# Optimization experiments

Measured on AMD Instinct MI355X. Metric: run time of the kernel, lower is better.

The kernel has to match this reference:

```python
import jax, jax.numpy as jnp
import numpy as np
from math import sqrt

BASE = 10000.0  # rope_theta
NUM_HEADS = 16


def _quant(x):
    # per-row (last-dim) symmetric int8 fake-quant, matching ActivationQuantSTE.forward
    scale = 127.0 / jnp.maximum(jnp.max(jnp.abs(x), axis=-1, keepdims=True), 1e-5)
    return jnp.clip(jnp.round(x * scale), -128.0, 127.0) / scale


@jax.custom_vjp
def act_quant(x):
    return _quant(x)

def _aq_fwd(x):
    return _quant(x), None

def _aq_bwd(_, g):
    return (g,)  # straight-through estimator

act_quant.defvjp(_aq_fwd, _aq_bwd)


def complex_linear(xr, xi, Wr, Wi):
    # ComplexLinearBase: quantize activations, then
    #   y_real = q_real @ Wr^T + q_imag @ Wi^T
    #   y_imag = q_real @ Wi^T - q_imag @ Wr^T
    qr = act_quant(xr)
    qi = act_quant(xi)
    yr = qr @ Wr.T + qi @ Wi.T
    yi = qr @ Wi.T - qi @ Wr.T
    return yr, yi


def setup_inputs() -> dict:
    T, H = 2048, 2048
    key = jax.random.key(0)
    ks = jax.random.split(key, 10)
    w = lambda k: jax.random.normal(k, (H, H), jnp.float32) * 0.02
    return {
        "hidden_real": jax.random.normal(ks[0], (T, H), jnp.float32),
        "hidden_imag": jax.random.normal(ks[1], (T, H), jnp.float32),
        "positions": jnp.arange(T, dtype=jnp.int32),
        "Wq_r": w(ks[2]), "Wq_i": w(ks[3]),
        "Wk_r": w(ks[4]), "Wk_i": w(ks[5]),
        "Wv_r": w(ks[6]), "Wv_i": w(ks[7]),
        "Wo_r": w(ks[8]), "Wo_i": w(ks[9]),
    }


def reference(hidden_real, hidden_imag, positions, Wq_r, Wq_i, Wk_r, Wk_i, Wv_r, Wv_i, Wo_r, Wo_i):
    T, H = hidden_real.shape
    NH = NUM_HEADS
    D = H // NH  # head_dim

    # complex QKV projections with int8 activation fake-quant
    qr, qi = complex_linear(hidden_real, hidden_imag, Wq_r, Wq_i)
    kr, ki = complex_linear(hidden_real, hidden_imag, Wk_r, Wk_i)
    vr, vi = complex_linear(hidden_real, hidden_imag, Wv_r, Wv_i)

    # Complex RoPE: interleaving (real, imag) then GPT-J-style rotation with
    # head_size = rotary_dim = 2*D is equivalent to rotating (real, imag) pairs:
    #   out_real = real*cos - imag*sin ; out_imag = imag*cos + real*sin
    # inv_freq = base^-(arange(0, 2D, 2)/(2D)) = base^-(arange(D)/D), len D.
    inv_freq = 1.0 / (BASE ** (jnp.arange(D, dtype=jnp.float32) / D))
    freqs = positions.astype(jnp.float32)[:, None] * inv_freq[None, :]  # [T, D]
    # cache is stored in bf16 in the original module
    cos = jnp.cos(freqs).astype(jnp.bfloat16).astype(jnp.float32)[:, None, :]  # [T,1,D]
    sin = jnp.sin(freqs).astype(jnp.bfloat16).astype(jnp.float32)[:, None, :]

    def rope(xr_, xi_):
        r = xr_.reshape(T, NH, D)
        i = xi_.reshape(T, NH, D)
        return r * cos - i * sin, i * cos + r * sin

    qr3, qi3 = rope(qr, qi)
    kr3, ki3 = rope(kr, ki)
    vr3 = vr.reshape(T, NH, D)
    vi3 = vi.reshape(T, NH, D)

    # causal attention; scores = Re(q . conj(k)) / sqrt(2*D)  (complex dim is 2*D)
    scale = 1.0 / sqrt(2 * D)
    scores = (jnp.einsum('thd,shd->hts', qr3, kr3)
              + jnp.einsum('thd,shd->hts', qi3, ki3)) * scale  # [NH, T, T]
    causal = jnp.tril(jnp.ones((T, T), dtype=bool))
    scores = jnp.where(causal[None], scores, -1e9)
    p = jax.nn.softmax(scores, axis=-1)

    out_r = jnp.einsum('hts,shd->thd', p, vr3).reshape(T, H)
    out_i = jnp.einsum('hts,shd->thd', p, vi3).reshape(T, H)

    # complex output projection (with activation fake-quant)
    return complex_linear(out_r, out_i, Wo_r, Wo_i)
```

## Files before the change

kernel.cpp:

```cpp
#include <hip/hip_runtime.h>


typedef float v4f __attribute__((ext_vector_type(4)));
typedef _Float16 v8h __attribute__((ext_vector_type(8)));
typedef _Float16 v4h __attribute__((ext_vector_type(4)));

typedef const __attribute__((address_space(1))) void glob_void;
typedef __attribute__((address_space(3))) void lds_void;

__device__ __forceinline__ void gload16(const _Float16* gp, _Float16* lp) {
  __builtin_amdgcn_global_load_lds((glob_void*)gp, (lds_void*)lp, 16, 0, 0);
}

__device__ __forceinline__ float bf16_rt(float f) {
  union { float f; unsigned u; } a; a.f = f;
  unsigned r = (a.u + 0x7fffu + ((a.u >> 16) & 1u)) & 0xffff0000u;
  union { unsigned u; float f; } b; b.u = r;
  return b.f;
}

#define EPI_QKV 0
#define EPI_OUT 1

#define SBAR()  __builtin_amdgcn_sched_barrier(0)
#define WBAR()  __builtin_amdgcn_s_barrier()
#define LGKM0() asm volatile("s_waitcnt lgkmcnt(0)" ::: "memory")

__global__ __launch_bounds__(512, 2) void gemm_qkv256(
    const _Float16* __restrict__ A, const _Float16* __restrict__ B,
    _Float16* __restrict__ Yq, _Float16* __restrict__ vt)
{
  const int p = blockIdx.x;
  const int xcd = p & 7, s = p >> 3;
  const int mt = s & 7, ntl = s >> 3;
  const int nt = xcd * 8 + ntl;
  const int m0 = mt << 8;
  const int n0 = nt * 192;

  __shared__ __align__(16) _Float16 lds[57344];

  const int tid = threadIdx.x, lane = tid & 63, wave = tid >> 6;
  const int quad = lane >> 4, l15 = lane & 15;
  const int wm = wave >> 2, wn = wave & 3;

  const int rr = tid >> 2;
  const int lc8 = (((tid & 3) ^ ((tid >> 3) & 3)) << 3);
  const _Float16* gA = A + (long long)(m0 + rr) * 4096 + lc8;
  const _Float16* gBj[3];
#pragma unroll
  for (int j = 0; j < 3; ++j) {
    const int ks = (j == 2) || (j == 1 && tid >= 256);
    const int r = j * 128 + (tid >> 2) - ks * 192;
    gBj[j] = B + (long long)(n0 + r) * 4096 + ks * 32 + lc8;
  }

  const int co = ((quad ^ ((l15 >> 1) & 3)) << 3);
  const int aBase = (wm * 128 + l15) * 32 + co;
  const int bBase = (wn * 48 + l15) * 32 + co;

  v4f acc[8][3] = {};

  {
    _Float16* sd = lds + tid * 8;
    gload16(gA, sd);
    gload16(gA + 524288, sd + 4096);
    gload16(gBj[0], sd + 16384);
    gload16(gBj[1], sd + 20480);
    gload16(gA + 32, sd + 8192);
    gload16(gA + 524288 + 32, sd + 12288);
    gload16(gBj[2], sd + 24576);
  }
  asm volatile("s_waitcnt vmcnt(3)" ::: "memory");
  WBAR();

  for (int t = 0; t < 64; ++t) {
    const _Float16* As = lds + (t & 1) * 28672;
    const _Float16* Bs = As + 16384;
    _Float16* sd = lds + ((t & 1) ^ 1) * 28672 + tid * 8;
    const int k1 = (t + 1) << 6;
    const bool stg = (t < 63);

    v8h bf[3], af[4];

    af[0] = *(const v8h*)&As[aBase];
    af[1] = *(const v8h*)&As[aBase + 512];
    af[2] = *(const v8h*)&As[aBase + 1024];
    af[3] = *(const v8h*)&As[aBase + 1536];
    bf[0] = *(const v8h*)&Bs[bBase];
    bf[1] = *(const v8h*)&Bs[bBase + 512];
    bf[2] = *(const v8h*)&Bs[bBase + 1024];
    if (stg) { gload16(gA + k1, sd); gload16(gA + k1 + 524288, sd + 4096); }
    SBAR(); WBAR(); LGKM0(); SBAR();
    __builtin_amdgcn_s_setprio(1);
#pragma unroll
    for (int i = 0; i < 4; ++i)
#pragma unroll
      for (int nf = 0; nf < 3; ++nf)
        acc[i][nf] = __builtin_amdgcn_mfma_f32_16x16x32_f16(af[i], bf[nf], acc[i][nf], 0, 0, 0);
    __builtin_amdgcn_s_setprio(0);
    WBAR();

    af[0] = *(const v8h*)&As[aBase + 2048];
    af[1] = *(const v8h*)&As[aBase + 2560];
    af[2] = *(const v8h*)&As[aBase + 3072];
    af[3] = *(const v8h*)&As[aBase + 3584];
    if (stg) { gload16(gBj[0] + k1, sd + 16384); gload16(gBj[1] + k1, sd + 20480); }
    SBAR(); WBAR(); LGKM0(); SBAR();
    __builtin_amdgcn_s_setprio(1);
#pragma unroll
    for (int i = 0; i < 4; ++i)
#pragma unroll
      for (int nf = 0; nf < 3; ++nf)
        acc[4 + i][nf] = __builtin_amdgcn_mfma_f32_16x16x32_f16(af[i], bf[nf], acc[4 + i][nf], 0, 0, 0);
    __builtin_amdgcn_s_setprio(0);
    if (stg) asm volatile("s_waitcnt vmcnt(4)" ::: "memory");
    else     asm volatile("s_waitcnt vmcnt(0)" ::: "memory");
    WBAR();

    bf[0] = *(const v8h*)&Bs[bBase + 6144];
    bf[1] = *(const v8h*)&Bs[bBase + 6656];
    bf[2] = *(const v8h*)&Bs[bBase + 7168];
    af[0] = *(const v8h*)&As[aBase + 8192];
    af[1] = *(const v8h*)&As[aBase + 8704];
    af[2] = *(const v8h*)&As[aBase + 9216];
    af[3] = *(const v8h*)&As[aBase + 9728];
    if (stg) { gload16(gA + k1 + 32, sd + 8192); gload16(gA + k1 + 524288 + 32, sd + 12288); }
    SBAR(); WBAR(); LGKM0(); SBAR();
    __builtin_amdgcn_s_setprio(1);
#pragma unroll
    for (int i = 0; i < 4; ++i)
#pragma unroll
      for (int nf = 0; nf < 3; ++nf)
        acc[i][nf] = __builtin_amdgcn_mfma_f32_16x16x32_f16(af[i], bf[nf], acc[i][nf], 0, 0, 0);
    __builtin_amdgcn_s_setprio(0);
    WBAR();

    af[0] = *(const v8h*)&As[aBase + 10240];
    af[1] = *(const v8h*)&As[aBase + 10752];
    af[2] = *(const v8h*)&As[aBase + 11264];
    af[3] = *(const v8h*)&As[aBase + 11776];
    if (stg) gload16(gBj[2] + k1, sd + 24576);
    SBAR(); WBAR(); LGKM0(); SBAR();
    __builtin_amdgcn_s_setprio(1);
#pragma unroll
    for (int i = 0; i < 4; ++i)
#pragma unroll
      for (int nf = 0; nf < 3; ++nf)
        acc[4 + i][nf] = __builtin_amdgcn_mfma_f32_16x16x32_f16(af[i], bf[nf], acc[4 + i][nf], 0, 0, 0);
    __builtin_amdgcn_s_setprio(0);
    if (stg) asm volatile("s_waitcnt vmcnt(3)" ::: "memory");
    WBAR();
  }

#pragma unroll
  for (int mf = 0; mf < 8; ++mf) {
#pragma unroll
    for (int nf = 0; nf < 3; ++nf) {
      const int col = n0 + wn * 48 + nf * 16 + l15;
      const int row0 = m0 + wm * 128 + mf * 16 + quad * 4;
      if (col >= 8192) {
        const int c = col - 8192;
        const int hh = (c & 2047) >> 7;
        const int dcol = (c < 2048) ? (c & 127) : (128 + (c & 127));
        v4h pk;
#pragma unroll
        for (int r = 0; r < 4; ++r) pk[r] = (_Float16)acc[mf][nf][r];
        *(v4h*)(vt + ((long long)(hh * 256 + dcol)) * 2048 + row0) = pk;
      } else {
#pragma unroll
        for (int r = 0; r < 4; ++r)
          Yq[(long long)(row0 + r) * 8192 + col] = (_Float16)acc[mf][nf][r];
      }
    }
  }
}

template<int EPI>
__global__ __launch_bounds__(256) void gemm_nt(
    const _Float16* __restrict__ A, const _Float16* __restrict__ B,
    void* __restrict__ Cv, int K, int lda, int ldb, int ldc,
    _Float16* __restrict__ vtout)
{
  const int m0 = blockIdx.x * 128, n0 = blockIdx.y * 128;

  __shared__ __align__(16) _Float16 As[128 * 32];
  __shared__ __align__(16) _Float16 Bs[128 * 32];

  const int tid = threadIdx.x, lane = tid & 63, wave = tid >> 6;
  const int off0 = tid * 8, off1 = 2048 + tid * 8;
  const int r0 = off0 >> 5, r1 = off1 >> 5;
  const int c0 = ((((off0 >> 3) & 3) ^ ((r0 >> 1) & 3)) << 3);
  const int c1 = ((((off1 >> 3) & 3) ^ ((r1 >> 1) & 3)) << 3);
  const _Float16* ga0 = A + (long long)(m0 + r0) * lda + c0;
  const _Float16* ga1 = A + (long long)(m0 + r1) * lda + c1;
  const _Float16* gb0 = B + (long long)(n0 + r0) * ldb + c0;
  const _Float16* gb1 = B + (long long)(n0 + r1) * ldb + c1;

  const int mr = (wave >> 1) * 64 + (lane & 15);
  const int nr = (wave & 1) * 64 + (lane & 15);
  const int kq = lane >> 4;

  v4f acc[4][4] = {};

  for (int k0 = 0; k0 < K; k0 += 32) {
    gload16(ga0 + k0, As + off0);
    gload16(ga1 + k0, As + off1);
    gload16(gb0 + k0, Bs + off0);
    gload16(gb1 + k0, Bs + off1);
    __syncthreads();
    v8h a[4], b[4];
#pragma unroll
    for (int i = 0; i < 4; ++i) {
      const int r = mr + i * 16;
      a[i] = *(const v8h*)&As[r * 32 + ((kq ^ ((r >> 1) & 3)) << 3)];
    }
#pragma unroll
    for (int j = 0; j < 4; ++j) {
      const int r = nr + j * 16;
      b[j] = *(const v8h*)&Bs[r * 32 + ((kq ^ ((r >> 1) & 3)) << 3)];
    }
#pragma unroll
    for (int i = 0; i < 4; ++i)
#pragma unroll
      for (int j = 0; j < 4; ++j)
        acc[i][j] = __builtin_amdgcn_mfma_f32_16x16x32_f16(a[i], b[j], acc[i][j], 0, 0, 0);
    __syncthreads();
  }

  const int cr = (wave >> 1) * 64 + (lane >> 4) * 4;
  const int cc = (wave & 1) * 64 + (lane & 15);
#pragma unroll
  for (int i = 0; i < 4; ++i)
#pragma unroll
    for (int j = 0; j < 4; ++j) {
      const int col = n0 + cc + j * 16;
      if (EPI == EPI_QKV && col >= 8192) {
        const int c = col - 8192;
        const int hh = (c & 2047) >> 7;
        const int dcol = (c < 2048) ? (c & 127) : (128 + (c & 127));
        const int row0 = m0 + cr + i * 16;
        v4h pk;
#pragma unroll
        for (int r = 0; r < 4; ++r) pk[r] = (_Float16)acc[i][j][r];
        *(v4h*)(vtout + ((long long)(hh * 256 + dcol)) * 2048 + row0) = pk;
      } else {
#pragma unroll
        for (int r = 0; r < 4; ++r) {
          const int row = m0 + cr + i * 16 + r;
          const float v = acc[i][j][r];
          if (EPI == EPI_QKV) {
            ((_Float16*)Cv)[(long long)row * ldc + col] = (_Float16)v;
          } else {
            float* O = (float*)Cv;
            if (col < 2048) O[(long long)row * 2048 + col] = v;
            else O[2048ll * 2048 + (long long)row * 2048 + (col - 2048)] = v;
          }
        }
      }
    }
}

__global__ __launch_bounds__(256) void quant_rows(
    const float* __restrict__ s0, const float* __restrict__ s1,
    _Float16* __restrict__ dst)
{
  const int t = blockIdx.x, y = blockIdx.y;
  const float* src = (y ? s1 : s0) + (long long)t * 2048;
  const int tid = threadIdx.x, lane = tid & 63, wave = tid >> 6;
  __shared__ float rbuf[4];
  const v4f a = *(const v4f*)(src + tid * 4);
  const v4f b = *(const v4f*)(src + 1024 + tid * 4);
  float m = 0.f;
#pragma unroll
  for (int k = 0; k < 4; ++k)
    m = fmaxf(m, fmaxf(fabsf(a[k]), fabsf(b[k])));
  for (int o = 1; o < 64; o <<= 1) m = fmaxf(m, __shfl_xor(m, o, 64));
  if (lane == 0) rbuf[wave] = m;
  __syncthreads();
  m = fmaxf(fmaxf(rbuf[0], rbuf[1]), fmaxf(rbuf[2], rbuf[3]));
  const float scale = 127.f / fmaxf(m, 1e-5f);
  const float inv = 1.f / scale;
  _Float16* d = dst + (long long)t * 4096 + (long long)y * 2048 + tid * 4;
  v4h qa, qb;
#pragma unroll
  for (int k = 0; k < 4; ++k) {
    qa[k] = (_Float16)(fminf(fmaxf(rintf(a[k] * scale), -128.f), 127.f) * inv);
    qb[k] = (_Float16)(fminf(fmaxf(rintf(b[k] * scale), -128.f), 127.f) * inv);
  }
  *(v4h*)d = qa;
  *(v4h*)(d + 1024) = qb;
}

__global__ __launch_bounds__(256) void wprep(
    const float* __restrict__ Wq_r, const float* __restrict__ Wq_i,
    const float* __restrict__ Wk_r, const float* __restrict__ Wk_i,
    const float* __restrict__ Wv_r, const float* __restrict__ Wv_i,
    const float* __restrict__ Wo_r, const float* __restrict__ Wo_i,
    _Float16* __restrict__ Bqkv, _Float16* __restrict__ Bo)
{
  const float* Ws[8] = {Wq_r, Wq_i, Wk_r, Wk_i, Wv_r, Wv_i, Wo_r, Wo_i};
  const int i = blockIdx.x * 256 + threadIdx.x;
  const int w = i >> 18;
  const int rem = i & 262143;
  const int j = rem >> 7;
  const int cb = (rem & 127) * 16;
  const float* src = Ws[w] + (long long)j * 2048 + cb;
  _Float16* Bp = (w < 6) ? (Bqkv + (long long)(w >> 1) * 4096 * 4096) : Bo;
  const int isI = w & 1;
  _Float16* d1 = Bp + (long long)j * 4096 + (isI ? 2048 + cb : cb);
  _Float16* d2 = Bp + (long long)(2048 + j) * 4096 + (isI ? cb : 2048 + cb);
  const float sg2 = isI ? 1.f : -1.f;
#pragma unroll
  for (int q = 0; q < 4; ++q) {
    const v4f v = *(const v4f*)(src + q * 4);
    v4h o1, o2;
#pragma unroll
    for (int k = 0; k < 4; ++k) {
      o1[k] = (_Float16)v[k];
      o2[k] = (_Float16)(v[k] * sg2);
    }
    *(v4h*)(d1 + q * 4) = o1;
    *(v4h*)(d2 + q * 4) = o2;
  }
}

__global__ __launch_bounds__(256) void trig_kernel(
    const int* __restrict__ pos, float* __restrict__ cs)
{
  const int t = blockIdx.x * 2 + (threadIdx.x >> 7);
  const int d = threadIdx.x & 127;
  const float invf = (float)pow(10000.0, -(double)d / 128.0);
  const float fr = (float)pos[t] * invf;
  const double fd = (double)fr;
  cs[((long long)t * 128 + d) * 2]     = bf16_rt((float)cos(fd));
  cs[((long long)t * 128 + d) * 2 + 1] = bf16_rt((float)sin(fd));
}

__global__ __launch_bounds__(256) void rope_kernel(
    const _Float16* __restrict__ Yq, const float* __restrict__ cs,
    _Float16* __restrict__ qc, _Float16* __restrict__ kc)
{
  const int idx = blockIdx.x * 256 + threadIdx.x;
  const int d0 = (idx & 15) * 8;
  const int h  = (idx >> 4) & 15;
  const int t  = idx >> 8;
  const _Float16* y = Yq + (long long)t * 8192 + h * 128 + d0;
  const v8h qr8 = *(const v8h*)(y);
  const v8h qi8 = *(const v8h*)(y + 2048);
  const v8h kr8 = *(const v8h*)(y + 4096);
  const v8h ki8 = *(const v8h*)(y + 6144);
  const float* cp = cs + ((long long)t * 128 + d0) * 2;
  v8h qro, qio, kro, kio;
#pragma unroll
  for (int u = 0; u < 8; ++u) {
    const float c = cp[u * 2], s = cp[u * 2 + 1];
    const float qr = (float)qr8[u], qi = (float)qi8[u];
    const float kr = (float)kr8[u], ki = (float)ki8[u];
    qro[u] = (_Float16)(qr * c - qi * s);
    qio[u] = (_Float16)(qi * c + qr * s);
    kro[u] = (_Float16)(kr * c - ki * s);
    kio[u] = (_Float16)(ki * c + kr * s);
  }
  _Float16* qo = qc + ((long long)h * 2048 + t) * 256 + d0;
  _Float16* ko = kc + ((long long)h * 2048 + t) * 256 + d0;
  *(v8h*)qo = qro; *(v8h*)(qo + 128) = qio;
  *(v8h*)ko = kro; *(v8h*)(ko + 128) = kio;
}

__global__ __launch_bounds__(256, 4) void flash_attn(
    const _Float16* __restrict__ qc, const _Float16* __restrict__ kc,
    const _Float16* __restrict__ vt, float* __restrict__ attn)
{
  __shared__ __align__(16) _Float16 Ps[32 * 72];
  __shared__ float pmax[2][32];
  __shared__ float psum[2][32];

  const int h  = blockIdx.y;
  const int qt = ((h >> 3) & 1) ? (63 - (int)blockIdx.x) : (int)blockIdx.x;
  const int q0 = qt * 32;
  const int tid = threadIdx.x, lane = tid & 63, wave = tid >> 6;
  const int mi = wave >> 1, ni = wave & 1;
  const int quad = lane >> 4, l15 = lane & 15;

  const _Float16* qh = qc + (long long)h * 2048 * 256;
  const _Float16* kh = kc + (long long)h * 2048 * 256;
  const _Float16* vh = vt + (long long)h * 256 * 2048;

  const _Float16 scl = (_Float16)0.09016844f;
  v8h qf[8];
  {
    const int t = q0 + mi * 16 + l15;
#pragma unroll
    for (int ks = 0; ks < 8; ++ks) {
      v8h q = *(const v8h*)(qh + (long long)t * 256 + ks * 32 + quad * 8);
#pragma unroll
      for (int u = 0; u < 8; ++u) q[u] *= scl;
      qf[ks] = q;
    }
  }

  float mrow[4], lrow[4];
  v4f acc_o[8];
#pragma unroll
  for (int r = 0; r < 4; ++r) { mrow[r] = -1e30f; lrow[r] = 0.f; }
#pragma unroll
  for (int nt = 0; nt < 8; ++nt) acc_o[nt] = (v4f){0.f, 0.f, 0.f, 0.f};

  const int stmax = qt >> 1;
  for (int st = 0; st <= stmax; ++st) {
    const int s0 = st * 64;

    v4f sa[2] = {};
#pragma unroll
    for (int ks = 0; ks < 8; ++ks) {
      v8h bk[2];
#pragma unroll
      for (int jn = 0; jn < 2; ++jn)
        bk[jn] = *(const v8h*)(kh + (long long)(s0 + ni * 32 + jn * 16 + l15) * 256
                               + ks * 32 + quad * 8);
#pragma unroll
      for (int jn = 0; jn < 2; ++jn)
        sa[jn] = __builtin_amdgcn_mfma_f32_16x16x32_f16(qf[ks], bk[jn], sa[jn], 0, 0, 0);
    }

    const bool diag = (st == stmax);
    float pm[4];
#pragma unroll
    for (int r = 0; r < 4; ++r) pm[r] = -1e30f;
#pragma unroll
    for (int jn = 0; jn < 2; ++jn)
#pragma unroll
      for (int r = 0; r < 4; ++r) {
        float v = sa[jn][r];
        if (diag) {
          const int rl = q0 + mi * 16 + quad * 4 + r;
          const int cl = s0 + ni * 32 + jn * 16 + l15;
          if (cl > rl) v = -1e30f;
        }
        sa[jn][r] = v;
        pm[r] = fmaxf(pm[r], v);
      }
#pragma unroll
    for (int o = 1; o < 16; o <<= 1)
#pragma unroll
      for (int r = 0; r < 4; ++r)
        pm[r] = fmaxf(pm[r], __shfl_xor(pm[r], o, 64));
    if (l15 == 0) {
#pragma unroll
      for (int r = 0; r < 4; ++r)
        pmax[ni][mi * 16 + quad * 4 + r] = pm[r];
    }
    __syncthreads();

    float al[4], ps[4];
#pragma unroll
    for (int r = 0; r < 4; ++r) {
      const int row = mi * 16 + quad * 4 + r;
      const float mn = fmaxf(mrow[r], fmaxf(pmax[0][row], pmax[1][row]));
      al[r] = __builtin_amdgcn_exp2f(mrow[r] - mn);
      mrow[r] = mn;
      ps[r] = 0.f;
    }
#pragma unroll
    for (int jn = 0; jn < 2; ++jn)
#pragma unroll
      for (int r = 0; r < 4; ++r) {
        const float e = __builtin_amdgcn_exp2f(sa[jn][r] - mrow[r]);
        ps[r] += e;
        Ps[(mi * 16 + quad * 4 + r) * 72 + ni * 32 + jn * 16 + l15] = (_Float16)e;
      }
#pragma unroll
    for (int o = 1; o < 16; o <<= 1)
#pragma unroll
      for (int r = 0; r < 4; ++r)
        ps[r] += __shfl_xor(ps[r], o, 64);
    if (l15 == 0) {
#pragma unroll
      for (int r = 0; r < 4; ++r)
        psum[ni][mi * 16 + quad * 4 + r] = ps[r];
    }
    __syncthreads();

#pragma unroll
    for (int r = 0; r < 4; ++r) {
      const int row = mi * 16 + quad * 4 + r;
      lrow[r] = lrow[r] * al[r] + psum[0][row] + psum[1][row];
    }
#pragma unroll
    for (int nt = 0; nt < 8; ++nt)
#pragma unroll
      for (int r = 0; r < 4; ++r)
        acc_o[nt][r] *= al[r];

#pragma unroll
    for (int kc2 = 0; kc2 < 2; ++kc2) {
      v8h pa;
      {
        const int row = mi * 16 + l15;
        pa = *(const v8h*)(Ps + row * 72 + kc2 * 32 + quad * 8);
      }
#pragma unroll
      for (int nt = 0; nt < 8; ++nt) {
        const v8h vb = *(const v8h*)(vh + (long long)(ni * 128 + nt * 16 + l15) * 2048
                                     + s0 + kc2 * 32 + quad * 8);
        acc_o[nt] = __builtin_amdgcn_mfma_f32_16x16x32_f16(pa, vb, acc_o[nt], 0, 0, 0);
      }
    }
  }

  float inv[4];
#pragma unroll
  for (int r = 0; r < 4; ++r) inv[r] = 1.f / lrow[r];
#pragma unroll
  for (int nt = 0; nt < 8; ++nt) {
    const int d = ni * 128 + nt * 16 + l15;
    float* dst = attn + ((d < 128) ? 0ll : (2048ll * 2048)) + (h * 128 + (d & 127));
#pragma unroll
    for (int r = 0; r < 4; ++r) {
      const int t = q0 + mi * 16 + quad * 4 + r;
      dst[(long long)t * 2048] = acc_o[nt][r] * inv[r];
    }
  }
}

extern "C" void kernel_launch(void* const* d_in, const int* in_sizes, int n_in,
                              void* d_out, int out_size, void* d_ws, size_t ws_size,
                              hipStream_t stream) {
  const float* hr   = (const float*)d_in[0];
  const float* hi   = (const float*)d_in[1];
  const int*   pos  = (const int*)d_in[2];
  const float* Wq_r = (const float*)d_in[3];
  const float* Wq_i = (const float*)d_in[4];
  const float* Wk_r = (const float*)d_in[5];
  const float* Wk_i = (const float*)d_in[6];
  const float* Wv_r = (const float*)d_in[7];
  const float* Wv_i = (const float*)d_in[8];
  const float* Wo_r = (const float*)d_in[9];
  const float* Wo_i = (const float*)d_in[10];

  char* ws = (char*)d_ws;
  _Float16* Bqkv = (_Float16*)(ws);
  float*    attn = (float*)   (ws);
  float*    cs   = (float*)   (ws + (32ll  << 20));
  _Float16* Bo   = (_Float16*)(ws + (96ll  << 20));
  _Float16* Ac   = (_Float16*)(ws + (128ll << 20));
  _Float16* Yq   = (_Float16*)(ws + (144ll << 20));
  _Float16* qc   = (_Float16*)(ws + (176ll << 20));
  _Float16* kc   = (_Float16*)(ws + (192ll << 20));
  _Float16* vt   = (_Float16*)(ws + (208ll << 20));

  quant_rows<<<dim3(2048, 2), 256, 0, stream>>>(hr, hi, Ac);
  wprep<<<8192, 256, 0, stream>>>(Wq_r, Wq_i, Wk_r, Wk_i, Wv_r, Wv_i, Wo_r, Wo_i, Bqkv, Bo);
  gemm_qkv256<<<512, 512, 0, stream>>>(Ac, Bqkv, Yq, vt);
  trig_kernel<<<1024, 256, 0, stream>>>(pos, cs);
  rope_kernel<<<2048, 256, 0, stream>>>(Yq, cs, qc, kc);
  flash_attn<<<dim3(64, 16), 256, 0, stream>>>(qc, kc, vt, attn);
  quant_rows<<<dim3(2048, 2), 256, 0, stream>>>(attn, attn + 2048ll * 2048, Ac);
  gemm_nt<EPI_OUT><<<dim3(16, 32), 256, 0, stream>>>(
      Ac, Bo, d_out, 4096, 4096, 4096, 0, nullptr);
}
```

Measured before the change: 838.9 us.

## Restructure flash attention so each wave owns full rows, removing block syncs

Flash attention now uses a 64-row query tile per block with each of the four waves owning 16 query rows across the full 64-key tile and all 256 head dims. This removes the cross-wave max/sum exchange through LDS and both __syncthreads per key tile, since row statistics are reduced within a wave. Each wave now issues twice the K loads and MFMAs per tile and holds 16 output accumulators, so register pressure rises and the occupancy hint drops from 4 to 2. The grid halves to 512 blocks. s_setprio hints are also added around the MFMA bursts.

```diff
diff --git a/kernel.cpp b/kernel.cpp
--- a/kernel.cpp
+++ b/kernel.cpp
@@ -367,29 +367,28 @@
   *(v8h*)ko = kro; *(v8h*)(ko + 128) = kio;
 }
 
-__global__ __launch_bounds__(256, 4) void flash_attn(
+__global__ __launch_bounds__(256, 2) void flash_attn(
     const _Float16* __restrict__ qc, const _Float16* __restrict__ kc,
     const _Float16* __restrict__ vt, float* __restrict__ attn)
 {
-  __shared__ __align__(16) _Float16 Ps[32 * 72];
-  __shared__ float pmax[2][32];
-  __shared__ float psum[2][32];
+  __shared__ __align__(16) _Float16 Ps[4][16][72];
 
   const int h  = blockIdx.y;
-  const int qt = ((h >> 3) & 1) ? (63 - (int)blockIdx.x) : (int)blockIdx.x;
-  const int q0 = qt * 32;
+  const int qt = ((h >> 3) & 1) ? (31 - (int)blockIdx.x) : (int)blockIdx.x;
+  const int q0 = qt * 64;
   const int tid = threadIdx.x, lane = tid & 63, wave = tid >> 6;
-  const int mi = wave >> 1, ni = wave & 1;
   const int quad = lane >> 4, l15 = lane & 15;
 
   const _Float16* qh = qc + (long long)h * 2048 * 256;
   const _Float16* kh = kc + (long long)h * 2048 * 256;
   const _Float16* vh = vt + (long long)h * 256 * 2048;
 
+  const int wrow = q0 + wave * 16;
+
   const _Float16 scl = (_Float16)0.09016844f;
   v8h qf[8];
   {
-    const int t = q0 + mi * 16 + l15;
+    const int t = wrow + l15;
 #pragma unroll
     for (int ks = 0; ks < 8; ++ks) {
       v8h q = *(const v8h*)(qh + (long long)t * 256 + ks * 32 + quad * 8);
@@ -400,41 +399,42 @@
   }
 
   float mrow[4], lrow[4];
-  v4f acc_o[8];
+  v4f acc_o[16];
 #pragma unroll
   for (int r = 0; r < 4; ++r) { mrow[r] = -1e30f; lrow[r] = 0.f; }
 #pragma unroll
-  for (int nt = 0; nt < 8; ++nt) acc_o[nt] = (v4f){0.f, 0.f, 0.f, 0.f};
-
-  const int stmax = qt >> 1;
-  for (int st = 0; st <= stmax; ++st) {
+  for (int nt = 0; nt < 16; ++nt) acc_o[nt] = (v4f){0.f, 0.f, 0.f, 0.f};
+
+  for (int st = 0; st <= qt; ++st) {
     const int s0 = st * 64;
-
-    v4f sa[2] = {};
+    const bool diag = (st == qt);
+
+    v4f sa[4] = {};
 #pragma unroll
     for (int ks = 0; ks < 8; ++ks) {
-      v8h bk[2];
-#pragma unroll
-      for (int jn = 0; jn < 2; ++jn)
-        bk[jn] = *(const v8h*)(kh + (long long)(s0 + ni * 32 + jn * 16 + l15) * 256
+      v8h bk[4];
+#pragma unroll
+      for (int jn = 0; jn < 4; ++jn)
+        bk[jn] = *(const v8h*)(kh + (long long)(s0 + jn * 16 + l15) * 256
                                + ks * 32 + quad * 8);
-#pragma unroll
-      for (int jn = 0; jn < 2; ++jn)
+      __builtin_amdgcn_s_setprio(1);
+#pragma unroll
+      for (int jn = 0; jn < 4; ++jn)
         sa[jn] = __builtin_amdgcn_mfma_f32_16x16x32_f16(qf[ks], bk[jn], sa[jn], 0, 0, 0);
-    }
-
-    const bool diag = (st == stmax);
+      __builtin_amdgcn_s_setprio(0);
+    }
+
     float pm[4];
 #pragma unroll
     for (int r = 0; r < 4; ++r) pm[r] = -1e30f;
 #pragma unroll
-    for (int jn = 0; jn < 2; ++jn)
+    for (int jn = 0; jn < 4; ++jn)
 #pragma unroll
       for (int r = 0; r < 4; ++r) {
         float v = sa[jn][r];
         if (diag) {
-          const int rl = q0 + mi * 16 + quad * 4 + r;
-          const int cl = s0 + ni * 32 + jn * 16 + l15;
+          const int rl = wrow + quad * 4 + r;
+          const int cl = s0 + jn * 16 + l15;
           if (cl > rl) v = -1e30f;
         }
         sa[jn][r] = v;
@@ -445,66 +445,48 @@
 #pragma unroll
       for (int r = 0; r < 4; ++r)
         pm[r] = fmaxf(pm[r], __shfl_xor(pm[r], o, 64));
-    if (l15 == 0) {
-#pragma unroll
-      for (int r = 0; r < 4; ++r)
-        pmax[ni][mi * 16 + quad * 4 + r] = pm[r];
-    }
-    __syncthreads();
 
     float al[4], ps[4];
 #pragma unroll
     for (int r = 0; r < 4; ++r) {
-      const int row = mi * 16 + quad * 4 + r;
-      const float mn = fmaxf(mrow[r], fmaxf(pmax[0][row], pmax[1][row]));
+      const float mn = fmaxf(mrow[r], pm[r]);
       al[r] = __builtin_amdgcn_exp2f(mrow[r] - mn);
       mrow[r] = mn;
       ps[r] = 0.f;
     }
 #pragma unroll
-    for (int jn = 0; jn < 2; ++jn)
+    for (int jn = 0; jn < 4; ++jn)
 #pragma unroll
       for (int r = 0; r < 4; ++r) {
         const float e = __builtin_amdgcn_exp2f(sa[jn][r] - mrow[r]);
         ps[r] += e;
-        Ps[(mi * 16 + quad * 4 + r) * 72 + ni * 32 + jn * 16 + l15] = (_Float16)e;
+        Ps[wave][quad * 4 + r][jn * 16 + l15] = (_Float16)e;
       }
 #pragma unroll
     for (int o = 1; o < 16; o <<= 1)
 #pragma unroll
       for (int r = 0; r < 4; ++r)
         ps[r] += __shfl_xor(ps[r], o, 64);
-    if (l15 == 0) {
-#pragma unroll
-      for (int r = 0; r < 4; ++r)
-        psum[ni][mi * 16 + quad * 4 + r] = ps[r];
-    }
-    __syncthreads();
-
-#pragma unroll
-    for (int r = 0; r < 4; ++r) {
-      const int row = mi * 16 + quad * 4 + r;
-      lrow[r] = lrow[r] * al[r] + psum[0][row] + psum[1][row];
-    }
-#pragma unroll
-    for (int nt = 0; nt < 8; ++nt)
+#pragma unroll
+    for (int r = 0; r < 4; ++r)
+      lrow[r] = lrow[r] * al[r] + ps[r];
+#pragma unroll
+    for (int nt = 0; nt < 16; ++nt)
 #pragma unroll
       for (int r = 0; r < 4; ++r)
         acc_o[nt][r] *= al[r];
 
 #pragma unroll
     for (int kc2 = 0; kc2 < 2; ++kc2) {
-      v8h pa;
-      {
-        const int row = mi * 16 + l15;
-        pa = *(const v8h*)(Ps + row * 72 + kc2 * 32 + quad * 8);
-      }
-#pragma unroll
-      for (int nt = 0; nt < 8; ++nt) {
-        const v8h vb = *(const v8h*)(vh + (long long)(ni * 128 + nt * 16 + l15) * 2048
+      const v8h pa = *(const v8h*)&Ps[wave][l15][kc2 * 32 + quad * 8];
+      __builtin_amdgcn_s_setprio(1);
+#pragma unroll
+      for (int nt = 0; nt < 16; ++nt) {
+        const v8h vb = *(const v8h*)(vh + (long long)(nt * 16 + l15) * 2048
                                      + s0 + kc2 * 32 + quad * 8);
         acc_o[nt] = __builtin_amdgcn_mfma_f32_16x16x32_f16(pa, vb, acc_o[nt], 0, 0, 0);
       }
+      __builtin_amdgcn_s_setprio(0);
     }
   }
 
@@ -512,12 +494,12 @@
 #pragma unroll
   for (int r = 0; r < 4; ++r) inv[r] = 1.f / lrow[r];
 #pragma unroll
-  for (int nt = 0; nt < 8; ++nt) {
-    const int d = ni * 128 + nt * 16 + l15;
+  for (int nt = 0; nt < 16; ++nt) {
+    const int d = nt * 16 + l15;
     float* dst = attn + ((d < 128) ? 0ll : (2048ll * 2048)) + (h * 128 + (d & 127));
 #pragma unroll
     for (int r = 0; r < 4; ++r) {
-      const int t = q0 + mi * 16 + quad * 4 + r;
+      const int t = wrow + quad * 4 + r;
       dst[(long long)t * 2048] = acc_o[nt][r] * inv[r];
     }
   }
@@ -554,7 +536,7 @@
   gemm_qkv256<<<512, 512, 0, stream>>>(Ac, Bqkv, Yq, vt);
   trig_kernel<<<1024, 256, 0, stream>>>(pos, cs);
   rope_kernel<<<2048, 256, 0, stream>>>(Yq, cs, qc, kc);
-  flash_attn<<<dim3(64, 16), 256, 0, stream>>>(qc, kc, vt, attn);
+  flash_attn<<<dim3(32, 16), 256, 0, stream>>>(qc, kc, vt, attn);
   quant_rows<<<dim3(2048, 2), 256, 0, stream>>>(attn, attn + 2048ll * 2048, Ac);
   gemm_nt<EPI_OUT><<<dim3(16, 32), 256, 0, stream>>>(
       Ac, Bo, d_out, 4096, 4096, 4096, 0, nullptr);
```

After: 885.4 us. +5.5%, slower.
